# Kernel optimization log

Hardware: AMD Instinct MI355X
Metric: run time of the kernel (lower is better)

Reference implementation:

```python
import jax, jax.numpy as jnp
import numpy as np

E = 1024
H = 16
D = E // H  # head dim 64
B = 2
S = 2048


def setup_inputs() -> dict:
    key = jax.random.key(0)
    k1, k2, k3, k4, k5 = jax.random.split(key, 5)
    scale = 1.0 / np.sqrt(E)
    return {
        "x": jax.random.normal(k1, (B, S, E), dtype=jnp.float32),
        "W_in": jax.random.normal(k2, (E, 3 * E), dtype=jnp.float32) * scale,
        "b_in": jnp.zeros((3 * E,), dtype=jnp.float32),
        "W_out": jax.random.normal(k3, (E, E), dtype=jnp.float32) * scale,
        "b_out": jnp.zeros((E,), dtype=jnp.float32),
        "causal_mask": 1,
    }


def reference(x, W_in, b_in, W_out, b_out, causal_mask):
    b, s, e = x.shape
    qkv = x @ W_in + b_in                      # [B,S,3E]
    q, k, v = jnp.split(qkv, 3, axis=-1)
    # [B,S,E] -> [B,H,S,D]
    q = q.reshape(b, s, H, D).transpose(0, 2, 1, 3)
    k = k.reshape(b, s, H, D).transpose(0, 2, 1, 3)
    v = v.reshape(b, s, H, D).transpose(0, 2, 1, 3)
    scores = jnp.einsum("bhqd,bhkd->bhqk", q, k)
    if causal_mask:
        # mask applied before scaling in the original; -inf is scale-invariant
        mask = jnp.triu(jnp.ones((s, s), dtype=bool), k=1)
        scores = jnp.where(mask, -jnp.inf, scores)
    scores = scores / np.sqrt(D)
    weight = jax.nn.softmax(scores, axis=-1)
    out = jnp.einsum("bhqk,bhkd->bhqd", weight, v)   # [B,H,S,D]
    out = out.transpose(0, 2, 1, 3).reshape(b, s, e)
    return out @ W_out + b_out
```

## Files before the change

### kernel.cpp

```cpp
#include <hip/hip_runtime.h>
#include <hip/hip_bf16.h>
#include <cmath>

typedef __bf16 bf16;
typedef __attribute__((ext_vector_type(8))) __bf16 bf16x8;
typedef __attribute__((ext_vector_type(4))) __bf16 bf16x4;
typedef __attribute__((ext_vector_type(4))) float f32x4;
typedef __attribute__((ext_vector_type(16))) float f32x16;
typedef unsigned int u32;

constexpr int S  = 2048;
constexpr int E  = 1024;
constexpr int H  = 16;
constexpr int D  = 64;
constexpr int B  = 2;
constexpr int M  = B * S;
constexpr int N3 = 3 * E;
constexpr int NROWS = B * H * S;

__constant__ int P_tab_d[16] = {1,1,1,1,1,2,2,2,2,2,2,3,3,3,3,3};
__constant__ int S_tab_d[16] = {0,1,2,3,4,5,7,9,11,13,15,17,20,23,26,29};
__constant__ int c_ord_d[32] = {15,15,10,10, 15,14,14,14,13,9,9,4,
                                13,13,12,12,8,8, 12,11,11,11,7,7,3,
                                6,6, 5,5,2, 1, 0};
__constant__ int p_ord_d[32] = {1,2,0,1, 0,0,1,2,2,0,1,0,
                                0,1,1,2,0,1, 0,0,1,2,0,1,0,
                                0,1, 0,1,0, 0, 0};

static __device__ __forceinline__ void gload16(const void* g, void* l) {
  __builtin_amdgcn_global_load_lds((const __attribute__((address_space(1))) void*)g,
                                   (__attribute__((address_space(3))) void*)l, 16, 0, 0);
}

static __device__ __forceinline__ u32 pack2(float a, float b) {
  union { bf16 h[2]; u32 u; } r;
  r.h[0] = (bf16)a; r.h[1] = (bf16)b;
  return r.u;
}
typedef union { u32 w[4]; bf16x8 v; } FU;

__global__ __launch_bounds__(256) void k_prep(
    const float* __restrict__ x, bf16* __restrict__ xb,
    const float* __restrict__ W_in, bf16* __restrict__ wtin,
    const float* __restrict__ W_out, bf16* __restrict__ wtout)
{
  const int bid = blockIdx.x;
  if (bid < 4096) {
    const int i = (bid * 256 + threadIdx.x) * 4;
    const float4 v = *(const float4*)(x + i);
    bf16x4 o = { (bf16)v.x, (bf16)v.y, (bf16)v.z, (bf16)v.w };
    *(bf16x4*)(xb + i) = o;
  } else {
    __shared__ float t[32][33];
    const float* in;
    bf16* out;
    int R, C, bx, by;
    if (bid < 4096 + 3072) {
      const int b = bid - 4096;
      in = W_in; out = wtin; R = E; C = N3;
      bx = b % (N3 / 32); by = b / (N3 / 32);
    } else {
      const int b = bid - 4096 - 3072;
      in = W_out; out = wtout; R = E; C = E;
      bx = b % (E / 32); by = b / (E / 32);
    }
    const int c0 = bx * 32, r0 = by * 32;
    const int tx = threadIdx.x & 31, ty = threadIdx.x >> 5;
    #pragma unroll
    for (int j = 0; j < 32; j += 8)
      t[ty + j][tx] = in[(size_t)(r0 + ty + j) * C + c0 + tx];
    __syncthreads();
    #pragma unroll
    for (int j = 0; j < 32; j += 8)
      out[(size_t)(c0 + ty + j) * R + r0 + tx] = (bf16)t[tx][ty + j];
  }
}

template<int EPI>
__global__ __launch_bounds__(256) void k_gemm(
    const bf16* __restrict__ A, const bf16* __restrict__ Bt,
    const float* __restrict__ bias, float* __restrict__ outF,
    bf16* __restrict__ oQ, bf16* __restrict__ oK, bf16* __restrict__ oV,
    int Kdim, int Nn)
{
  __shared__ __align__(16) char smem[65536];
  const int tid = threadIdx.x;
  const int lane = tid & 63, w = tid >> 6;
  const int lane15 = lane & 15, quad = lane >> 4;
  const int wm = w >> 1, wn = w & 1;

  const int nbx = Nn >> 7;
  const int nwg = gridDim.x;
  const int bid = blockIdx.x;
  const int swz = (bid & 7) * (nwg >> 3) + (bid >> 3);
  const int bn0 = (swz % nbx) * 128;
  const int bm0 = (swz / nbx) * 128;

  const int so0 = w * 1024 + lane * 16;
  int srow[4], slk[4];
  #pragma unroll
  for (int p = 0; p < 4; ++p) {
    const int o = p * 4096 + so0;
    const int row = o >> 7, cbyte = o & 127;
    srow[p] = row;
    slk[p] = (cbyte ^ ((row & 7) << 4)) >> 1;
  }

  f32x4 acc[4][4] = {};
  const int nkt = Kdim >> 6;

  #pragma unroll
  for (int p = 0; p < 4; ++p) {
    gload16(A  + (size_t)(bm0 + srow[p]) * Kdim + slk[p], smem +         p * 4096 + w * 1024);
    gload16(Bt + (size_t)(bn0 + srow[p]) * Kdim + slk[p], smem + 32768 + p * 4096 + w * 1024);
  }

  #pragma unroll 1
  for (int kt = 0; kt < nkt; ++kt) {
    const int cur = kt & 1;
    __builtin_amdgcn_s_barrier();
    if (kt + 1 < nkt) {
      const int k0 = (kt + 1) << 6;
      const int nb = (cur ^ 1) * 16384;
      #pragma unroll
      for (int p = 0; p < 4; ++p) {
        gload16(A  + (size_t)(bm0 + srow[p]) * Kdim + k0 + slk[p],
                smem + nb +         p * 4096 + w * 1024);
        gload16(Bt + (size_t)(bn0 + srow[p]) * Kdim + k0 + slk[p],
                smem + nb + 32768 + p * 4096 + w * 1024);
      }
      asm volatile("s_waitcnt vmcnt(8)" ::: "memory");
    } else {
      asm volatile("s_waitcnt vmcnt(0)" ::: "memory");
    }
    __builtin_amdgcn_s_barrier();

    const char* cA = smem + cur * 16384;
    const char* cB = smem + 32768 + cur * 16384;
    #pragma unroll
    for (int kk = 0; kk < 2; ++kk) {
      bf16x8 af[4], bfr[4];
      #pragma unroll
      for (int f = 0; f < 4; ++f) {
        const int ra = wm * 64 + f * 16 + lane15;
        af[f] = *(const bf16x8*)(cA + ra * 128 +
                 ((kk * 64 + (quad << 4)) ^ ((ra & 7) << 4)));
        const int rb = wn * 64 + f * 16 + lane15;
        bfr[f] = *(const bf16x8*)(cB + rb * 128 +
                 ((kk * 64 + (quad << 4)) ^ ((rb & 7) << 4)));
      }
      #pragma unroll
      for (int i = 0; i < 4; ++i)
        #pragma unroll
        for (int j = 0; j < 4; ++j)
          acc[i][j] = __builtin_amdgcn_mfma_f32_16x16x32_bf16(af[i], bfr[j], acc[i][j], 0, 0, 0);
    }
  }

  if constexpr (EPI == 1) {
    #pragma unroll
    for (int i = 0; i < 4; ++i)
      #pragma unroll
      for (int j = 0; j < 4; ++j) {
        const int n = bn0 + wn * 64 + j * 16 + lane15;
        const float bv = bias[n];
        #pragma unroll
        for (int r = 0; r < 4; ++r) {
          const int m = bm0 + wm * 64 + i * 16 + quad * 4 + r;
          outF[(size_t)m * E + n] = acc[i][j][r] + bv;
        }
      }
  } else {
    const int which = bn0 >> 10;
    const int b  = bm0 >> 11;
    const int s0 = bm0 & (S - 1);
    const int cn0 = bn0 & (E - 1);
    if (which < 2) {
      __builtin_amdgcn_s_barrier();
      char* lC = smem;
      #pragma unroll
      for (int j = 0; j < 4; ++j) {
        const int n_loc = wn * 64 + j * 16 + lane15;
        const float bv = bias[bn0 + n_loc];
        #pragma unroll
        for (int i = 0; i < 4; ++i)
          #pragma unroll
          for (int r = 0; r < 4; ++r) {
            const int m_loc = wm * 64 + i * 16 + quad * 4 + r;
            *(bf16*)(lC + m_loc * 256 + ((n_loc * 2) ^ ((m_loc & 7) << 4))) =
                (bf16)(acc[i][j][r] + bv);
          }
      }
      __builtin_amdgcn_s_barrier();
      const int h0 = cn0 >> 6;
      #pragma unroll
      for (int it = 0; it < 8; ++it) {
        const int cch = w * 64 + it * 8 + (lane >> 3);
        const int m_loc = cch >> 1, hh = cch & 1, piece = lane & 7;
        const bf16x8 vv = *(const bf16x8*)(lC + m_loc * 256 +
                          ((hh * 128 + piece * 16) ^ ((m_loc & 7) << 4)));
        if (which == 0) {
          *(bf16x8*)(oQ + ((size_t)(b * H + h0 + hh) * S + s0 + m_loc) * D + piece * 8) = vv;
        } else {
          const size_t hb = (size_t)(b * H + h0 + hh) * S * D;
          const int tile = (s0 + m_loc) >> 6;
          const int row = m_loc & 63;
          *(bf16x8*)(oK + hb + (size_t)tile * 4096 + (piece >> 1) * 1024 +
                     (row >> 5) * 512 + (32 * (piece & 1) + (row & 31)) * 8) = vv;
        }
      }
    } else {
      #pragma unroll
      for (int j = 0; j < 4; ++j) {
        const int n_loc = wn * 64 + j * 16 + lane15;
        const int cn = cn0 + n_loc;
        const int hv = cn >> 6, dd = cn & 63;
        const float bv = bias[bn0 + n_loc];
        const size_t hb = (size_t)(b * H + hv) * S * D;
        #pragma unroll
        for (int i = 0; i < 4; ++i) {
          const int scol_g = s0 + wm * 64 + i * 16 + quad * 4;
          const int vtile = scol_g >> 6;
          const int cg = (scol_g & 63) >> 3;
          bf16x4 pk = { (bf16)(acc[i][j][0] + bv), (bf16)(acc[i][j][1] + bv),
                        (bf16)(acc[i][j][2] + bv), (bf16)(acc[i][j][3] + bv) };
          *(bf16x4*)(oV + hb + (size_t)vtile * 4096 + (cg >> 1) * 1024 +
                     (dd >> 5) * 512 + (32 * (cg & 1) + (dd & 31)) * 8 +
                     (quad & 1) * 4) = pk;
        }
      }
    }
  }
}

__global__ __launch_bounds__(256) void k_attn(
    const bf16* __restrict__ Qb, const bf16* __restrict__ Kf, const bf16* __restrict__ Vf,
    bf16* __restrict__ pO0, bf16* __restrict__ pO1,
    float* __restrict__ pM, float* __restrict__ pL, const int* __restrict__ cmask)
{
  __shared__ float corr_lds[4][32];
  __shared__ float lrow_lds[4][32];

  const int tid = threadIdx.x, lane = tid & 63, w = tid >> 6;
  const int h = lane >> 5, q31 = lane & 31;
  const int bh = blockIdx.x;
  const int yy = blockIdx.y;
  const int c  = c_ord_d[yy];
  const int p  = p_ord_d[yy];
  const int Pc = P_tab_d[c];
  const int sslot = S_tab_d[c] + p;
  const int causal = cmask[0];
  const float S2 = 0.18033688011112042f;

  const bf16* Qh = Qb + (size_t)bh * S * D;
  const bf16* Kh = Kf + (size_t)bh * S * D;
  const bf16* Vh = Vf + (size_t)bh * S * D;

  const int nt = causal ? (2 * c + 2) : (S / 64);
  const int t0 = (p * nt) / Pc;
  const int t1 = ((p + 1) * nt) / Pc;
  const int q0w = c * 128 + 32 * w;
  const int qg  = q0w + q31;
  const int t1w = causal ? min(t1, ((q0w + 31) >> 6) + 1) : t1;

  bf16x8 qf[4];
  #pragma unroll
  for (int ds = 0; ds < 4; ++ds)
    qf[ds] = *(const bf16x8*)(Qh + (size_t)qg * D + 16 * ds + 8 * h);

  f32x16 o0 = {}, o1 = {};
  float mrun = -INFINITY, lr = 0.f;

  bf16x8 kc0[4], kc1[4];
  {
    const bf16* ktb = Kh + (size_t)t0 * 4096;
    #pragma unroll
    for (int ds = 0; ds < 4; ++ds) {
      kc0[ds] = *(const bf16x8*)(ktb + ds * 1024 +       lane * 8);
      kc1[ds] = *(const bf16x8*)(ktb + ds * 1024 + 512 + lane * 8);
    }
  }

  #pragma unroll 1
  for (int t = t0; t < t1w; ++t) {
    const bf16* vtb = Vh + (size_t)t * 4096;

    f32x16 s0v = {}, s1v = {};
    __builtin_amdgcn_s_setprio(1);
    #pragma unroll
    for (int ds = 0; ds < 4; ++ds) {
      s0v = __builtin_amdgcn_mfma_f32_32x32x16_bf16(kc0[ds], qf[ds], s0v, 0, 0, 0);
      s1v = __builtin_amdgcn_mfma_f32_32x32x16_bf16(kc1[ds], qf[ds], s1v, 0, 0, 0);
    }
    __builtin_amdgcn_s_setprio(0);

    bf16x8 vf0[4], vf1[4];
    #pragma unroll
    for (int ks = 0; ks < 4; ++ks) {
      vf0[ks] = *(const bf16x8*)(vtb + ks * 1024 +       lane * 8);
      vf1[ks] = *(const bf16x8*)(vtb + ks * 1024 + 512 + lane * 8);
    }
    if (t + 1 < t1w) {
      const bf16* ktb2 = Kh + (size_t)(t + 1) * 4096;
      #pragma unroll
      for (int ds = 0; ds < 4; ++ds) {
        kc0[ds] = *(const bf16x8*)(ktb2 + ds * 1024 +       lane * 8);
        kc1[ds] = *(const bf16x8*)(ktb2 + ds * 1024 + 512 + lane * 8);
      }
    }

    if (causal && (64 * t + 63 > q0w)) {
      #pragma unroll
      for (int rr = 0; rr < 16; ++rr) {
        const int kg = 64 * t + (rr & 3) + 8 * (rr >> 2) + 4 * h;
        if (kg > qg)      s0v[rr] = -INFINITY;
        if (kg + 32 > qg) s1v[rr] = -INFINITY;
      }
    }

    float a8[8];
    #pragma unroll
    for (int i = 0; i < 8; ++i)
      a8[i] = fmaxf(fmaxf(s0v[i], s0v[i + 8]), fmaxf(s1v[i], s1v[i + 8]));
    float tmax = fmaxf(fmaxf(fmaxf(a8[0], a8[1]), fmaxf(a8[2], a8[3])),
                       fmaxf(fmaxf(a8[4], a8[5]), fmaxf(a8[6], a8[7])));
    tmax = fmaxf(tmax, __shfl_xor(tmax, 32, 64));

    const bool nogrow = __all(tmax <= mrun);
    const float mnew = nogrow ? mrun : fmaxf(mrun, tmax);
    float corrf = 1.f;
    if (!nogrow) {
      corrf = __builtin_amdgcn_exp2f((mrun - mnew) * S2);
      corr_lds[w][q31] = corrf;
    }
    const float msc = mnew * S2;

    #pragma unroll
    for (int rr = 0; rr < 16; ++rr) {
      s0v[rr] = __builtin_amdgcn_exp2f(__builtin_fmaf(s0v[rr], S2, -msc));
      s1v[rr] = __builtin_amdgcn_exp2f(__builtin_fmaf(s1v[rr], S2, -msc));
    }

    float b8[8];
    #pragma unroll
    for (int i = 0; i < 8; ++i)
      b8[i] = (s0v[i] + s0v[i + 8]) + (s1v[i] + s1v[i + 8]);
    float psum = ((b8[0] + b8[1]) + (b8[2] + b8[3])) + ((b8[4] + b8[5]) + (b8[6] + b8[7]));
    psum += __shfl_xor(psum, 32, 64);
    lr = lr * corrf + psum;
    mrun = mnew;

    u32 pk[8][2];
    #pragma unroll
    for (int jj = 0; jj < 4; ++jj) {
      pk[jj][0]     = pack2(s0v[4 * jj],     s0v[4 * jj + 1]);
      pk[jj][1]     = pack2(s0v[4 * jj + 2], s0v[4 * jj + 3]);
      pk[jj + 4][0] = pack2(s1v[4 * jj],     s1v[4 * jj + 1]);
      pk[jj + 4][1] = pack2(s1v[4 * jj + 2], s1v[4 * jj + 3]);
    }

    if (!nogrow) {
      #pragma unroll
      for (int j = 0; j < 4; ++j) {
        const f32x4 cv = *(const f32x4*)&corr_lds[w][8 * j + 4 * h];
        #pragma unroll
        for (int sr = 0; sr < 4; ++sr) {
          o0[4 * j + sr] *= cv[sr];
          o1[4 * j + sr] *= cv[sr];
        }
      }
    }

    __builtin_amdgcn_s_setprio(1);
    #pragma unroll
    for (int ks = 0; ks < 4; ++ks) {
      u32 a0 = pk[2 * ks][0], b0 = pk[2 * ks + 1][0];
      u32 a1 = pk[2 * ks][1], b1 = pk[2 * ks + 1][1];
      asm volatile("v_permlane32_swap_b32 %0, %1" : "+v"(a0), "+v"(b0));
      asm volatile("v_permlane32_swap_b32 %0, %1" : "+v"(a1), "+v"(b1));
      FU f; f.w[0] = a0; f.w[1] = a1; f.w[2] = b0; f.w[3] = b1;
      o0 = __builtin_amdgcn_mfma_f32_32x32x16_bf16(f.v, vf0[ks], o0, 0, 0, 0);
      o1 = __builtin_amdgcn_mfma_f32_32x32x16_bf16(f.v, vf1[ks], o1, 0, 0, 0);
    }
    __builtin_amdgcn_s_setprio(0);
  }

  const int slotbase = ((bh & 15) * 32 + sslot) * 128;
  if (h == 0) {
    pM[(size_t)(bh * 32 + sslot) * 128 + 32 * w + q31] = mrun;
    pL[(size_t)(bh * 32 + sslot) * 128 + 32 * w + q31] = lr;
  }
  lrow_lds[w][q31] = lr;
  bf16* po = (bh < 16 ? pO0 : pO1) + (size_t)slotbase * D;
  #pragma unroll
  for (int j = 0; j < 4; ++j) {
    const f32x4 lv = *(const f32x4*)&lrow_lds[w][8 * j + 4 * h];
    #pragma unroll
    for (int sr = 0; sr < 4; ++sr) {
      const int rr = 4 * j + sr;
      const float inv = lv[sr] > 0.f ? 1.0f / lv[sr] : 0.f;
      const int qloc = 32 * w + (rr & 3) + 8 * (rr >> 2) + 4 * h;
      bf16* dst = po + (size_t)qloc * D;
      dst[q31]      = (bf16)(o0[rr] * inv);
      dst[32 + q31] = (bf16)(o1[rr] * inv);
    }
  }
}

__global__ __launch_bounds__(256) void k_combine(
    const bf16* __restrict__ pO0, const bf16* __restrict__ pO1,
    const float* __restrict__ pM, const float* __restrict__ pL,
    bf16* __restrict__ AO)
{
  const float S2 = 0.18033688011112042f;
  const int idx = blockIdx.x * 256 + threadIdx.x;
  const int row = idx >> 3, d0 = (idx & 7) * 8;
  const int bh = row >> 11, s = row & 2047;
  const int c = s >> 7, local = s & 127;
  const int Pc = P_tab_d[c], Sc = S_tab_d[c];
  const bf16* pbase = (bh < 16 ? pO0 : pO1);

  float mv[3], lv[3];
  float m = -INFINITY;
  #pragma unroll
  for (int p = 0; p < 3; ++p) {
    if (p < Pc) {
      mv[p] = pM[(size_t)(bh * 32 + Sc + p) * 128 + local];
      lv[p] = pL[(size_t)(bh * 32 + Sc + p) * 128 + local];
      m = fmaxf(m, mv[p]);
    }
  }
  float wsum = 0.f, wv[3];
  #pragma unroll
  for (int p = 0; p < 3; ++p) {
    wv[p] = 0.f;
    if (p < Pc && lv[p] > 0.f) {
      wv[p] = lv[p] * __builtin_amdgcn_exp2f((mv[p] - m) * S2);
      wsum += wv[p];
    }
  }
  const float inv = 1.0f / wsum;
  float acc[8] = {};
  #pragma unroll
  for (int p = 0; p < 3; ++p) {
    if (p < Pc) {
      const bf16x8 a = *(const bf16x8*)(pbase +
          ((size_t)((bh & 15) * 32 + Sc + p) * 128 + local) * D + d0);
      #pragma unroll
      for (int i = 0; i < 8; ++i)
        acc[i] += wv[p] * (float)a[i];
    }
  }
  bf16x8 o;
  #pragma unroll
  for (int i = 0; i < 8; ++i)
    o[i] = (bf16)(acc[i] * inv);
  const int bb = row >> 15, hh = (row >> 11) & 15;
  *(bf16x8*)(AO + ((size_t)(bb * S + s)) * E + hh * D + d0) = o;
}

extern "C" void kernel_launch(void* const* d_in, const int* in_sizes, int n_in,
                              void* d_out, int out_size, void* d_ws, size_t ws_size,
                              hipStream_t stream) {
  (void)in_sizes; (void)n_in; (void)out_size; (void)ws_size;
  const float* x     = (const float*)d_in[0];
  const float* W_in  = (const float*)d_in[1];
  const float* b_in  = (const float*)d_in[2];
  const float* W_out = (const float*)d_in[3];
  const float* b_out = (const float*)d_in[4];
  const int*   cmask = (const int*)d_in[5];

  char* ws = (char*)d_ws;
  bf16* xb    = (bf16*)ws; ws += (size_t)M * E * 2;
  bf16* wtin  = (bf16*)ws; ws += (size_t)N3 * E * 2;
  bf16* wtout = (bf16*)ws; ws += (size_t)E * E * 2;
  bf16* qB    = (bf16*)ws; ws += (size_t)B * H * S * D * 2;
  bf16* kF    = (bf16*)ws; ws += (size_t)B * H * S * D * 2;
  bf16* vF    = (bf16*)ws; ws += (size_t)B * H * S * D * 2;
  bf16* ao    = (bf16*)ws; ws += (size_t)M * E * 2;
  bf16* pO1   = (bf16*)ws; ws += (size_t)NROWS * D * 2;
  float* pMb  = (float*)ws; ws += (size_t)2 * NROWS * 4;
  float* pLb  = (float*)ws; ws += (size_t)2 * NROWS * 4;
  bf16* pO0   = xb;

  k_prep<<<4096 + 3072 + 1024, 256, 0, stream>>>(x, xb, W_in, wtin, W_out, wtout);
  k_gemm<0><<<dim3((M / 128) * (N3 / 128)), 256, 0, stream>>>(
      xb, wtin, b_in, nullptr, qB, kF, vF, E, N3);
  k_attn<<<dim3(32, 32), 256, 0, stream>>>(qB, kF, vF, pO0, pO1, pMb, pLb, cmask);
  k_combine<<<NROWS * 8 / 256, 256, 0, stream>>>(pO0, pO1, pMb, pLb, ao);
  k_gemm<1><<<dim3((M / 128) * (E / 128)), 256, 0, stream>>>(
      ao, wtout, b_out, (float*)d_out, nullptr, nullptr, nullptr, E, E);
}
```

Baseline: 110.4 us.

## Process 128-key tiles per attention iteration and rebalance split schedule

The attention inner loop now handles two 64-key K/V tiles per iteration, with four score accumulators. This halves the number of online-softmax max/rescale steps, and the skip-rescale test is relaxed so the running max is only updated when the tile max exceeds it by more than a fixed margin. The K/V register prefetch and the per-warp causal tile trimming are removed. The work-split tables are rebuilt for 30 slots instead of 32, and the grid shrinks to match. This trades fewer softmax reductions and launches for more register pressure, and more wasted masked work on diagonal tiles.

```diff
diff --git a/kernel.cpp b/kernel.cpp
--- a/kernel.cpp
+++ b/kernel.cpp
@@ -18,14 +18,12 @@
 constexpr int N3 = 3 * E;
 constexpr int NROWS = B * H * S;
 
-__constant__ int P_tab_d[16] = {1,1,1,1,1,2,2,2,2,2,2,3,3,3,3,3};
-__constant__ int S_tab_d[16] = {0,1,2,3,4,5,7,9,11,13,15,17,20,23,26,29};
-__constant__ int c_ord_d[32] = {15,15,10,10, 15,14,14,14,13,9,9,4,
-                                13,13,12,12,8,8, 12,11,11,11,7,7,3,
-                                6,6, 5,5,2, 1, 0};
-__constant__ int p_ord_d[32] = {1,2,0,1, 0,0,1,2,2,0,1,0,
-                                0,1,1,2,0,1, 0,0,1,2,0,1,0,
-                                0,1, 0,1,0, 0, 0};
+__constant__ int P_tab_d[16] = {1,1,1,1,1,1,2,2,2,2,2,2,3,3,3,3};
+__constant__ int S_tab_d[16] = {0,1,2,3,4,5,6,8,10,12,14,16,18,21,24,27};
+__constant__ int c_ord_d[30] = {15,11,11,10,5, 15,15,14,14,14,13,13,12,10,9,9,8,4,
+                                13,12,12,8,7,7,6,3, 6,2, 1, 0};
+__constant__ int p_ord_d[30] = {2,0,1,1,0, 0,1,0,1,2,1,2,2,0,0,1,1,0,
+                                0,0,1,0,0,1,1,0, 0,0, 0, 0};
 
 static __device__ __forceinline__ void gload16(const void* g, void* l) {
   __builtin_amdgcn_global_load_lds((const __attribute__((address_space(1))) void*)g,
@@ -256,12 +254,11 @@
   const bf16* Kh = Kf + (size_t)bh * S * D;
   const bf16* Vh = Vf + (size_t)bh * S * D;
 
-  const int nt = causal ? (2 * c + 2) : (S / 64);
+  const int nt = causal ? (c + 1) : (S / 128);
   const int t0 = (p * nt) / Pc;
   const int t1 = ((p + 1) * nt) / Pc;
   const int q0w = c * 128 + 32 * w;
   const int qg  = q0w + q31;
-  const int t1w = causal ? min(t1, ((q0w + 31) >> 6) + 1) : t1;
 
   bf16x8 qf[4];
   #pragma unroll
@@ -271,62 +268,52 @@
   f32x16 o0 = {}, o1 = {};
   float mrun = -INFINITY, lr = 0.f;
 
-  bf16x8 kc0[4], kc1[4];
-  {
-    const bf16* ktb = Kh + (size_t)t0 * 4096;
+  #pragma unroll 1
+  for (int t = t0; t < t1; ++t) {
+    const bf16* ktbA = Kh + (size_t)(2 * t) * 4096;
+    const bf16* ktbB = ktbA + 4096;
+    const bf16* vtbA = Vh + (size_t)(2 * t) * 4096;
+    const bf16* vtbB = vtbA + 4096;
+
+    f32x16 s0v = {}, s1v = {}, s2v = {}, s3v = {};
+    __builtin_amdgcn_s_setprio(1);
     #pragma unroll
     for (int ds = 0; ds < 4; ++ds) {
-      kc0[ds] = *(const bf16x8*)(ktb + ds * 1024 +       lane * 8);
-      kc1[ds] = *(const bf16x8*)(ktb + ds * 1024 + 512 + lane * 8);
-    }
-  }
-
-  #pragma unroll 1
-  for (int t = t0; t < t1w; ++t) {
-    const bf16* vtb = Vh + (size_t)t * 4096;
-
-    f32x16 s0v = {}, s1v = {};
-    __builtin_amdgcn_s_setprio(1);
+      const bf16x8 ka0 = *(const bf16x8*)(ktbA + ds * 1024 +       lane * 8);
+      const bf16x8 ka1 = *(const bf16x8*)(ktbA + ds * 1024 + 512 + lane * 8);
+      s0v = __builtin_amdgcn_mfma_f32_32x32x16_bf16(ka0, qf[ds], s0v, 0, 0, 0);
+      s1v = __builtin_amdgcn_mfma_f32_32x32x16_bf16(ka1, qf[ds], s1v, 0, 0, 0);
+    }
     #pragma unroll
     for (int ds = 0; ds < 4; ++ds) {
-      s0v = __builtin_amdgcn_mfma_f32_32x32x16_bf16(kc0[ds], qf[ds], s0v, 0, 0, 0);
-      s1v = __builtin_amdgcn_mfma_f32_32x32x16_bf16(kc1[ds], qf[ds], s1v, 0, 0, 0);
+      const bf16x8 kb0 = *(const bf16x8*)(ktbB + ds * 1024 +       lane * 8);
+      const bf16x8 kb1 = *(const bf16x8*)(ktbB + ds * 1024 + 512 + lane * 8);
+      s2v = __builtin_amdgcn_mfma_f32_32x32x16_bf16(kb0, qf[ds], s2v, 0, 0, 0);
+      s3v = __builtin_amdgcn_mfma_f32_32x32x16_bf16(kb1, qf[ds], s3v, 0, 0, 0);
     }
     __builtin_amdgcn_s_setprio(0);
 
-    bf16x8 vf0[4], vf1[4];
-    #pragma unroll
-    for (int ks = 0; ks < 4; ++ks) {
-      vf0[ks] = *(const bf16x8*)(vtb + ks * 1024 +       lane * 8);
-      vf1[ks] = *(const bf16x8*)(vtb + ks * 1024 + 512 + lane * 8);
-    }
-    if (t + 1 < t1w) {
-      const bf16* ktb2 = Kh + (size_t)(t + 1) * 4096;
-      #pragma unroll
-      for (int ds = 0; ds < 4; ++ds) {
-        kc0[ds] = *(const bf16x8*)(ktb2 + ds * 1024 +       lane * 8);
-        kc1[ds] = *(const bf16x8*)(ktb2 + ds * 1024 + 512 + lane * 8);
-      }
-    }
-
-    if (causal && (64 * t + 63 > q0w)) {
+    if (causal && (128 * t + 127 > q0w)) {
       #pragma unroll
       for (int rr = 0; rr < 16; ++rr) {
-        const int kg = 64 * t + (rr & 3) + 8 * (rr >> 2) + 4 * h;
+        const int kg = 128 * t + (rr & 3) + 8 * (rr >> 2) + 4 * h;
         if (kg > qg)      s0v[rr] = -INFINITY;
         if (kg + 32 > qg) s1v[rr] = -INFINITY;
+        if (kg + 64 > qg) s2v[rr] = -INFINITY;
+        if (kg + 96 > qg) s3v[rr] = -INFINITY;
       }
     }
 
     float a8[8];
     #pragma unroll
     for (int i = 0; i < 8; ++i)
-      a8[i] = fmaxf(fmaxf(s0v[i], s0v[i + 8]), fmaxf(s1v[i], s1v[i + 8]));
+      a8[i] = fmaxf(fmaxf(fmaxf(s0v[i], s0v[i + 8]), fmaxf(s1v[i], s1v[i + 8])),
+                    fmaxf(fmaxf(s2v[i], s2v[i + 8]), fmaxf(s3v[i], s3v[i + 8])));
     float tmax = fmaxf(fmaxf(fmaxf(a8[0], a8[1]), fmaxf(a8[2], a8[3])),
                        fmaxf(fmaxf(a8[4], a8[5]), fmaxf(a8[6], a8[7])));
     tmax = fmaxf(tmax, __shfl_xor(tmax, 32, 64));
 
-    const bool nogrow = __all(tmax <= mrun);
+    const bool nogrow = __all(tmax <= mrun + 64.f);
     const float mnew = nogrow ? mrun : fmaxf(mrun, tmax);
     float corrf = 1.f;
     if (!nogrow) {
@@ -339,24 +326,31 @@
     for (int rr = 0; rr < 16; ++rr) {
       s0v[rr] = __builtin_amdgcn_exp2f(__builtin_fmaf(s0v[rr], S2, -msc));
       s1v[rr] = __builtin_amdgcn_exp2f(__builtin_fmaf(s1v[rr], S2, -msc));
+      s2v[rr] = __builtin_amdgcn_exp2f(__builtin_fmaf(s2v[rr], S2, -msc));
+      s3v[rr] = __builtin_amdgcn_exp2f(__builtin_fmaf(s3v[rr], S2, -msc));
     }
 
     float b8[8];
     #pragma unroll
     for (int i = 0; i < 8; ++i)
-      b8[i] = (s0v[i] + s0v[i + 8]) + (s1v[i] + s1v[i + 8]);
+      b8[i] = ((s0v[i] + s0v[i + 8]) + (s1v[i] + s1v[i + 8])) +
+              ((s2v[i] + s2v[i + 8]) + (s3v[i] + s3v[i + 8]));
     float psum = ((b8[0] + b8[1]) + (b8[2] + b8[3])) + ((b8[4] + b8[5]) + (b8[6] + b8[7]));
     psum += __shfl_xor(psum, 32, 64);
     lr = lr * corrf + psum;
     mrun = mnew;
 
-    u32 pk[8][2];
+    u32 pkA[8][2], pkB[8][2];
     #pragma unroll
     for (int jj = 0; jj < 4; ++jj) {
-      pk[jj][0]     = pack2(s0v[4 * jj],     s0v[4 * jj + 1]);
-      pk[jj][1]     = pack2(s0v[4 * jj + 2], s0v[4 * jj + 3]);
-      pk[jj + 4][0] = pack2(s1v[4 * jj],     s1v[4 * jj + 1]);
-      pk[jj + 4][1] = pack2(s1v[4 * jj + 2], s1v[4 * jj + 3]);
+      pkA[jj][0]     = pack2(s0v[4 * jj],     s0v[4 * jj + 1]);
+      pkA[jj][1]     = pack2(s0v[4 * jj + 2], s0v[4 * jj + 3]);
+      pkA[jj + 4][0] = pack2(s1v[4 * jj],     s1v[4 * jj + 1]);
+      pkA[jj + 4][1] = pack2(s1v[4 * jj + 2], s1v[4 * jj + 3]);
+      pkB[jj][0]     = pack2(s2v[4 * jj],     s2v[4 * jj + 1]);
+      pkB[jj][1]     = pack2(s2v[4 * jj + 2], s2v[4 * jj + 3]);
+      pkB[jj + 4][0] = pack2(s3v[4 * jj],     s3v[4 * jj + 1]);
+      pkB[jj + 4][1] = pack2(s3v[4 * jj + 2], s3v[4 * jj + 3]);
     }
 
     if (!nogrow) {
@@ -374,13 +368,27 @@
     __builtin_amdgcn_s_setprio(1);
     #pragma unroll
     for (int ks = 0; ks < 4; ++ks) {
-      u32 a0 = pk[2 * ks][0], b0 = pk[2 * ks + 1][0];
-      u32 a1 = pk[2 * ks][1], b1 = pk[2 * ks + 1][1];
+      u32 a0 = pkA[2 * ks][0], b0 = pkA[2 * ks + 1][0];
+      u32 a1 = pkA[2 * ks][1], b1 = pkA[2 * ks + 1][1];
       asm volatile("v_permlane32_swap_b32 %0, %1" : "+v"(a0), "+v"(b0));
       asm volatile("v_permlane32_swap_b32 %0, %1" : "+v"(a1), "+v"(b1));
       FU f; f.w[0] = a0; f.w[1] = a1; f.w[2] = b0; f.w[3] = b1;
-      o0 = __builtin_amdgcn_mfma_f32_32x32x16_bf16(f.v, vf0[ks], o0, 0, 0, 0);
-      o1 = __builtin_amdgcn_mfma_f32_32x32x16_bf16(f.v, vf1[ks], o1, 0, 0, 0);
+      const bf16x8 vf0 = *(const bf16x8*)(vtbA + ks * 1024 +       lane * 8);
+      const bf16x8 vf1 = *(const bf16x8*)(vtbA + ks * 1024 + 512 + lane * 8);
+      o0 = __builtin_amdgcn_mfma_f32_32x32x16_bf16(f.v, vf0, o0, 0, 0, 0);
+      o1 = __builtin_amdgcn_mfma_f32_32x32x16_bf16(f.v, vf1, o1, 0, 0, 0);
+    }
+    #pragma unroll
+    for (int ks = 0; ks < 4; ++ks) {
+      u32 a0 = pkB[2 * ks][0], b0 = pkB[2 * ks + 1][0];
+      u32 a1 = pkB[2 * ks][1], b1 = pkB[2 * ks + 1][1];
+      asm volatile("v_permlane32_swap_b32 %0, %1" : "+v"(a0), "+v"(b0));
+      asm volatile("v_permlane32_swap_b32 %0, %1" : "+v"(a1), "+v"(b1));
+      FU f; f.w[0] = a0; f.w[1] = a1; f.w[2] = b0; f.w[3] = b1;
+      const bf16x8 vf0 = *(const bf16x8*)(vtbB + ks * 1024 +       lane * 8);
+      const bf16x8 vf1 = *(const bf16x8*)(vtbB + ks * 1024 + 512 + lane * 8);
+      o0 = __builtin_amdgcn_mfma_f32_32x32x16_bf16(f.v, vf0, o0, 0, 0, 0);
+      o1 = __builtin_amdgcn_mfma_f32_32x32x16_bf16(f.v, vf1, o1, 0, 0, 0);
     }
     __builtin_amdgcn_s_setprio(0);
   }
@@ -486,7 +494,7 @@
   k_prep<<<4096 + 3072 + 1024, 256, 0, stream>>>(x, xb, W_in, wtin, W_out, wtout);
   k_gemm<0><<<dim3((M / 128) * (N3 / 128)), 256, 0, stream>>>(
       xb, wtin, b_in, nullptr, qB, kF, vF, E, N3);
-  k_attn<<<dim3(32, 32), 256, 0, stream>>>(qB, kF, vF, pO0, pO1, pMb, pLb, cmask);
+  k_attn<<<dim3(32, 30), 256, 0, stream>>>(qB, kF, vF, pO0, pO1, pMb, pLb, cmask);
   k_combine<<<NROWS * 8 / 256, 256, 0, stream>>>(pO0, pO1, pMb, pLb, ao);
   k_gemm<1><<<dim3((M / 128) * (E / 128)), 256, 0, stream>>>(
       ao, wtout, b_out, (float*)d_out, nullptr, nullptr, nullptr, E, E);
```

After: 118.9 us. +7.7%, slower.

## Drop K prefetch and load V just-in-time to raise attention occupancy

Applied to the files above, without the earlier changes.

Removes the software prefetch of the next K tile and the early load of the full V tile. K is now loaded at the top of each iteration and V fragments are loaded right before each PV MFMA. Launch bounds now request 4 blocks per CU. The aim is to cut VGPR pressure so more waves are resident and can hide memory latency, at the cost of exposing the global load latency within each wave.

```diff
diff --git a/kernel.cpp b/kernel.cpp
--- a/kernel.cpp
+++ b/kernel.cpp
@@ -233,7 +233,7 @@
   }
 }
 
-__global__ __launch_bounds__(256) void k_attn(
+__global__ __launch_bounds__(256, 4) void k_attn(
     const bf16* __restrict__ Qb, const bf16* __restrict__ Kf, const bf16* __restrict__ Vf,
     bf16* __restrict__ pO0, bf16* __restrict__ pO1,
     float* __restrict__ pM, float* __restrict__ pL, const int* __restrict__ cmask)
@@ -271,43 +271,26 @@
   f32x16 o0 = {}, o1 = {};
   float mrun = -INFINITY, lr = 0.f;
 
-  bf16x8 kc0[4], kc1[4];
-  {
-    const bf16* ktb = Kh + (size_t)t0 * 4096;
-    #pragma unroll
-    for (int ds = 0; ds < 4; ++ds) {
-      kc0[ds] = *(const bf16x8*)(ktb + ds * 1024 +       lane * 8);
-      kc1[ds] = *(const bf16x8*)(ktb + ds * 1024 + 512 + lane * 8);
-    }
-  }
-
   #pragma unroll 1
   for (int t = t0; t < t1w; ++t) {
+    const bf16* ktb = Kh + (size_t)t * 4096;
     const bf16* vtb = Vh + (size_t)t * 4096;
+
+    bf16x8 kf0[4], kf1[4];
+    #pragma unroll
+    for (int ds = 0; ds < 4; ++ds) {
+      kf0[ds] = *(const bf16x8*)(ktb + ds * 1024 +       lane * 8);
+      kf1[ds] = *(const bf16x8*)(ktb + ds * 1024 + 512 + lane * 8);
+    }
 
     f32x16 s0v = {}, s1v = {};
     __builtin_amdgcn_s_setprio(1);
     #pragma unroll
     for (int ds = 0; ds < 4; ++ds) {
-      s0v = __builtin_amdgcn_mfma_f32_32x32x16_bf16(kc0[ds], qf[ds], s0v, 0, 0, 0);
-      s1v = __builtin_amdgcn_mfma_f32_32x32x16_bf16(kc1[ds], qf[ds], s1v, 0, 0, 0);
+      s0v = __builtin_amdgcn_mfma_f32_32x32x16_bf16(kf0[ds], qf[ds], s0v, 0, 0, 0);
+      s1v = __builtin_amdgcn_mfma_f32_32x32x16_bf16(kf1[ds], qf[ds], s1v, 0, 0, 0);
     }
     __builtin_amdgcn_s_setprio(0);
-
-    bf16x8 vf0[4], vf1[4];
-    #pragma unroll
-    for (int ks = 0; ks < 4; ++ks) {
-      vf0[ks] = *(const bf16x8*)(vtb + ks * 1024 +       lane * 8);
-      vf1[ks] = *(const bf16x8*)(vtb + ks * 1024 + 512 + lane * 8);
-    }
-    if (t + 1 < t1w) {
-      const bf16* ktb2 = Kh + (size_t)(t + 1) * 4096;
-      #pragma unroll
-      for (int ds = 0; ds < 4; ++ds) {
-        kc0[ds] = *(const bf16x8*)(ktb2 + ds * 1024 +       lane * 8);
-        kc1[ds] = *(const bf16x8*)(ktb2 + ds * 1024 + 512 + lane * 8);
-      }
-    }
 
     if (causal && (64 * t + 63 > q0w)) {
       #pragma unroll
@@ -379,8 +362,10 @@
       asm volatile("v_permlane32_swap_b32 %0, %1" : "+v"(a0), "+v"(b0));
       asm volatile("v_permlane32_swap_b32 %0, %1" : "+v"(a1), "+v"(b1));
       FU f; f.w[0] = a0; f.w[1] = a1; f.w[2] = b0; f.w[3] = b1;
-      o0 = __builtin_amdgcn_mfma_f32_32x32x16_bf16(f.v, vf0[ks], o0, 0, 0, 0);
-      o1 = __builtin_amdgcn_mfma_f32_32x32x16_bf16(f.v, vf1[ks], o1, 0, 0, 0);
+      const bf16x8 vf0 = *(const bf16x8*)(vtb + ks * 1024 +       lane * 8);
+      const bf16x8 vf1 = *(const bf16x8*)(vtb + ks * 1024 + 512 + lane * 8);
+      o0 = __builtin_amdgcn_mfma_f32_32x32x16_bf16(f.v, vf0, o0, 0, 0, 0);
+      o1 = __builtin_amdgcn_mfma_f32_32x32x16_bf16(f.v, vf1, o1, 0, 0, 0);
     }
     __builtin_amdgcn_s_setprio(0);
   }
```

Result: faster. 106.0 us (-4.0%).
